# Optimization experiments

Hardware: AMD Instinct MI355X
Metric: run time of the kernel (lower is better)

## Reference

```python
import jax, jax.numpy as jnp
import numpy as np

NUM_USERS = 200000
NUM_ARTISTS = 50000
LATENT_DIM = 64
NUM_EDGES = 2000000
NUM_LAYERS = 3


def setup_inputs() -> dict:
    key = jax.random.key(0)
    k_u, k_a, k_src, k_dst = jax.random.split(key, 4)
    x_users = jax.random.normal(k_u, (NUM_USERS, LATENT_DIM), dtype=jnp.float32)
    x_artists = jax.random.normal(k_a, (NUM_ARTISTS, LATENT_DIM), dtype=jnp.float32)
    # a2u: row 0 = artist (source) ids, row 1 = user (target) ids
    art = jax.random.randint(k_src, (NUM_EDGES,), 0, NUM_ARTISTS, dtype=jnp.int32)
    usr = jax.random.randint(k_dst, (NUM_EDGES,), 0, NUM_USERS, dtype=jnp.int32)
    edge_index_a2u = jnp.stack([art, usr], axis=0)
    # u2a is the reversed edge list: row 0 = user (source), row 1 = artist (target)
    edge_index_u2a = jnp.stack([usr, art], axis=0)
    return {
        "x_users": x_users,
        "x_artists": x_artists,
        "edge_index_a2u": edge_index_a2u,
        "edge_index_u2a": edge_index_u2a,
    }


def _scatter_mean(src_nodes, edge_index, dim_size):
    """Gather src_nodes[edge_index[0]] and scatter-mean onto edge_index[1].

    Matches torch_scatter.scatter(reduce='mean'): empty segments yield 0.
    """
    msgs = src_nodes[edge_index[0]]                     # [E, D] gather
    sums = jax.ops.segment_sum(msgs, edge_index[1], num_segments=dim_size)
    ones = jnp.ones((edge_index.shape[1],), dtype=src_nodes.dtype)
    counts = jax.ops.segment_sum(ones, edge_index[1], num_segments=dim_size)
    return sums / jnp.maximum(counts, 1.0)[:, None]


def reference(x_users, x_artists, edge_index_a2u, edge_index_u2a):
    scale = 1.0 / (NUM_LAYERS + 1)
    final_u = x_users * scale
    final_a = x_artists * scale
    for _ in range(NUM_LAYERS):
        x_users = _scatter_mean(x_artists, edge_index_a2u, NUM_USERS)
        x_artists = _scatter_mean(x_users, edge_index_u2a, NUM_ARTISTS)
        final_u = final_u + x_users * scale
        final_a = final_a + x_artists * scale
    return final_u, final_a
```

## Files before the change

### kernel.cpp

```cpp
#include <hip/hip_runtime.h>
#include <hip/hip_fp16.h>

#define D 64
#define TB 256

#define BSHIFT_U 10
#define BSHIFT_A 8
#define CAP   12288
#define CAP_P 16384
#define SENT  0xFFFFFFFFu
#define TSHIFT 14

typedef _Float16 half8 __attribute__((ext_vector_type(8)));
typedef float float8 __attribute__((ext_vector_type(8)));
typedef float f32x4 __attribute__((ext_vector_type(4)));

__device__ __forceinline__ float8 h8_to_f8(half8 h) {
    return __builtin_convertvector(h, float8);
}
template <typename T>
__device__ __forceinline__ T ntl(const T* p) { return __builtin_nontemporal_load(p); }
template <typename T>
__device__ __forceinline__ void nts(T* p, T v) { __builtin_nontemporal_store(v, p); }

__global__ __launch_bounds__(TB) void cvt_f16_zero_kernel(const f32x4* __restrict__ in,
                                                          half8* __restrict__ out, int n8,
                                                          int* __restrict__ bcur, int nb) {
    int i = blockIdx.x * blockDim.x + threadIdx.x;
    int stride = gridDim.x * blockDim.x;
    for (int j = i; j < nb; j += stride) bcur[j] = 0;
    for (int j = i; j < n8; j += stride) {
        f32x4 a = in[j * 2 + 0];
        f32x4 b = in[j * 2 + 1];
        half8 h;
        h[0] = (_Float16)a[0]; h[1] = (_Float16)a[1]; h[2] = (_Float16)a[2]; h[3] = (_Float16)a[3];
        h[4] = (_Float16)b[0]; h[5] = (_Float16)b[1]; h[6] = (_Float16)b[2]; h[7] = (_Float16)b[3];
        out[j] = h;
    }
}

__global__ __launch_bounds__(TB) void partition_both_kernel(const int* __restrict__ art,
                                                            const int* __restrict__ usr, int E,
                                                            int* __restrict__ bcur_u,
                                                            int* __restrict__ bcur_a,
                                                            unsigned* __restrict__ part_u,
                                                            unsigned* __restrict__ part_a,
                                                            int NBu, int NBa) {
    __shared__ int cu[256], bu[256], ca[256], ba[256];
    for (int i = threadIdx.x; i < NBu; i += TB) cu[i] = 0;
    for (int i = threadIdx.x; i < NBa; i += TB) ca[i] = 0;
    __syncthreads();
    int chunk = (E + gridDim.x - 1) / gridDim.x;
    int e0 = blockIdx.x * chunk;
    int e1 = min(E, e0 + chunk);
    for (int e = e0 + threadIdx.x; e < e1; e += TB) {
        atomicAdd(&cu[usr[e] >> BSHIFT_U], 1);
        atomicAdd(&ca[art[e] >> BSHIFT_A], 1);
    }
    __syncthreads();
    for (int i = threadIdx.x; i < NBu; i += TB) {
        int c = cu[i];
        bu[i] = c ? (i * CAP_P + atomicAdd(&bcur_u[i], (c + 15) & ~15)) : 0;
        cu[i] = 0;
    }
    for (int i = threadIdx.x; i < NBa; i += TB) {
        int c = ca[i];
        ba[i] = c ? (i * CAP_P + atomicAdd(&bcur_a[i], (c + 15) & ~15)) : 0;
        ca[i] = 0;
    }
    __syncthreads();
    for (int e = e0 + threadIdx.x; e < e1; e += TB) {
        int a = art[e];
        int u = usr[e];
        int bui = u >> BSHIFT_U;
        int lu = atomicAdd(&cu[bui], 1);
        part_u[bu[bui] + lu] = ((unsigned)a << BSHIFT_U) | ((unsigned)u & ((1u << BSHIFT_U) - 1u));
        int bai = a >> BSHIFT_A;
        int la = atomicAdd(&ca[bai], 1);
        part_a[ba[bai] + la] = ((unsigned)u << BSHIFT_A) | ((unsigned)a & ((1u << BSHIFT_A) - 1u));
    }
    __syncthreads();
    for (int i = threadIdx.x; i < NBu; i += TB) {
        int c = cu[i];
        if (c) {
            int pad = (c + 15) & ~15;
            for (int k = c; k < pad; ++k) part_u[bu[i] + k] = SENT;
        }
    }
    for (int i = threadIdx.x; i < NBa; i += TB) {
        int c = ca[i];
        if (c) {
            int pad = (c + 15) & ~15;
            for (int k = c; k < pad; ++k) part_a[ba[i] + k] = SENT;
        }
    }
}

template <int NPB, int NB, int BSHIFT>
__device__ __forceinline__ void local_csr_body(const unsigned* __restrict__ part,
                                               int ecount, int ebeg_p, int ebeg_c, int n0,
                                               int2* __restrict__ rowdeg,
                                               int* __restrict__ csr, int N,
                                               int* cnt, int* sdata) {
    const int tid = threadIdx.x;
    const int NBINS = NPB * NB;
    const int eend = ebeg_p + ecount;
    const unsigned mask = (unsigned)(NPB - 1);
    for (int i = tid; i < NBINS; i += TB) cnt[i] = 0;
    __syncthreads();
    for (int e = ebeg_p + tid; e < eend; e += TB) {
        unsigned r = part[e];
        if (r != SENT) {
            int bin = (int)(r & mask) * NB + (int)((r >> BSHIFT) >> TSHIFT);
            atomicAdd(&cnt[bin], 1);
        }
    }
    __syncthreads();
    const int ITEMS = NBINS / TB;
    const int ib = tid * ITEMS;
    int local = 0;
    for (int k = 0; k < ITEMS; ++k) local += cnt[ib + k];
    sdata[tid] = local;
    __syncthreads();
    for (int off = 1; off < TB; off <<= 1) {
        int t = (tid >= off) ? sdata[tid - off] : 0;
        __syncthreads();
        if (tid >= off) sdata[tid] += t;
        __syncthreads();
    }
    int run = sdata[tid] - local;
    const int NPT = ITEMS / NB;
    for (int j = 0; j < NPT; ++j) {
        const int nodeStart = run;
        int d = 0;
        for (int k = 0; k < NB; ++k) {
            int idx = ib + j * NB + k;
            int v = cnt[idx];
            cnt[idx] = run;
            run += v;
            d += v;
        }
        int n = n0 + (ib / NB) + j;
        if (n < N) rowdeg[n] = make_int2(ebeg_c + nodeStart, d);
    }
    __syncthreads();
    for (int e = ebeg_p + tid; e < eend; e += TB) {
        unsigned r = part[e];
        if (r == SENT) continue;
        int bin = (int)(r & mask) * NB + (int)((r >> BSHIFT) >> TSHIFT);
        int pos = atomicAdd(&cnt[bin], 1);
        csr[ebeg_c + pos] = (int)(r >> BSHIFT);
    }
}

__global__ __launch_bounds__(TB) void local_csr_both_kernel(const unsigned* __restrict__ part_u,
                                                            const unsigned* __restrict__ part_a,
                                                            const int* __restrict__ bcur_u,
                                                            const int* __restrict__ bcur_a,
                                                            int2* __restrict__ rowdeg_u,
                                                            int2* __restrict__ rowdeg_a,
                                                            int* __restrict__ csr_u,
                                                            int* __restrict__ csr_a,
                                                            int NU, int NA, int NBu) {
    __shared__ int cnt[4096];
    __shared__ int sdata[TB];
    const int b = blockIdx.x;
    if (b < NBu) {
        local_csr_body<1024, 4, BSHIFT_U>(part_u, bcur_u[b], b * CAP_P, b * CAP,
                                          b << BSHIFT_U, rowdeg_u, csr_u, NU, cnt, sdata);
    } else {
        const int bb = b - NBu;
        local_csr_body<256, 16, BSHIFT_A>(part_a, bcur_a[bb], bb * CAP_P, bb * CAP,
                                          bb << BSHIFT_A, rowdeg_a, csr_a, NA, cnt, sdata);
    }
}

__global__ __launch_bounds__(TB) void gather_mean_kernel(const half8* __restrict__ src,
                                                         const int* __restrict__ csr,
                                                         const int2* __restrict__ rowdeg,
                                                         half8* __restrict__ x_out,
                                                         f32x4* __restrict__ final_acc,
                                                         const f32x4* __restrict__ init_src,
                                                         const f32x4* __restrict__ fin_in0,
                                                         const half8* __restrict__ fin_x1,
                                                         const half8* __restrict__ fin_x2,
                                                         f32x4* __restrict__ fin_out,
                                                         int N, float scale) {
    const int lane = threadIdx.x & 7;
    int g = (blockIdx.x * blockDim.x + threadIdx.x) >> 3;
    const int ngroups = (gridDim.x * blockDim.x) >> 3;
    for (int n = g; n < N; n += ngroups) {
        const int2 rd = rowdeg[n];
        const int beg = rd.x;
        const int dg = rd.y;
        const int end = beg + dg;
        float8 a0 = 0.f, a1 = 0.f, a2 = 0.f, a3 = 0.f;
        int e = beg;
        for (; e + 4 <= end; e += 4) {
            const int s0 = csr[e + 0];
            const int s1 = csr[e + 1];
            const int s2 = csr[e + 2];
            const int s3 = csr[e + 3];
            a0 += h8_to_f8(src[s0 * 8 + lane]);
            a1 += h8_to_f8(src[s1 * 8 + lane]);
            a2 += h8_to_f8(src[s2 * 8 + lane]);
            a3 += h8_to_f8(src[s3 * 8 + lane]);
        }
        for (; e < end; ++e)
            a0 += h8_to_f8(src[csr[e] * 8 + lane]);
        float8 s = (a0 + a1) + (a2 + a3);
        const float inv = 1.f / (float)(dg > 0 ? dg : 1);
        float8 x = s * inv;
        const int o8 = n * 8 + lane;
        if (x_out != nullptr) {
            half8 h;
            for (int k = 0; k < 8; ++k) h[k] = (_Float16)x[k];
            x_out[o8] = h;
        }
        const int fo = n * (D / 4) + lane * 2;
        if (fin_out != nullptr) {
            float8 t = h8_to_f8(ntl(&fin_x1[o8])) + h8_to_f8(ntl(&fin_x2[o8])) + x;
            f32x4 f0 = ntl(&fin_in0[fo + 0]);
            f32x4 f1 = ntl(&fin_in0[fo + 1]);
            f32x4 t0 = {t[0], t[1], t[2], t[3]};
            f32x4 t1 = {t[4], t[5], t[6], t[7]};
            nts(&fin_out[fo + 0], (f0 + t0) * scale);
            nts(&fin_out[fo + 1], (f1 + t1) * scale);
        }
        if (final_acc != nullptr) {
            f32x4 f0, f1;
            if (init_src != nullptr) {
                f0 = init_src[fo + 0] * scale;
                f1 = init_src[fo + 1] * scale;
            } else {
                f0 = final_acc[fo + 0];
                f1 = final_acc[fo + 1];
            }
            f32x4 x0 = {x[0], x[1], x[2], x[3]};
            f32x4 x1 = {x[4], x[5], x[6], x[7]};
            final_acc[fo + 0] = f0 + x0 * scale;
            final_acc[fo + 1] = f1 + x1 * scale;
        }
    }
}

extern "C" void kernel_launch(void* const* d_in, const int* in_sizes, int n_in,
                              void* d_out, int out_size, void* d_ws, size_t ws_size,
                              hipStream_t stream) {
    const float* x_users   = (const float*)d_in[0];
    const float* x_artists = (const float*)d_in[1];
    const int*   a2u       = (const int*)d_in[2];

    const int NU = in_sizes[0] / D;
    const int NA = in_sizes[1] / D;
    const int E  = in_sizes[2] / 2;
    const int* art = a2u;
    const int* usr = a2u + E;

    const float scale = 0.25f;

    const int NBu = (NU + (1 << BSHIFT_U) - 1) >> BSHIFT_U;
    const int NBa = (NA + (1 << BSHIFT_A) - 1) >> BSHIFT_A;

    char* w = (char*)d_ws;
    size_t off = 0;
    auto alloc = [&](size_t bytes) -> char* {
        char* p = w + off;
        off += (bytes + 255) & ~(size_t)255;
        return p;
    };
    int2* rowdeg_u = (int2*)alloc((size_t)NU * 8);
    int2* rowdeg_a = (int2*)alloc((size_t)NA * 8);
    int* bcur      = (int*)alloc((size_t)(NBu + NBa) * 4);
    int* bcur_u    = bcur;
    int* bcur_a    = bcur + NBu;
    int* csr_u     = (int*)alloc((size_t)NBu * CAP * 4);
    int* csr_a     = (int*)alloc((size_t)NBa * CAP * 4);
    half8* xa_in   = (half8*)alloc((size_t)NA * D * 2);
    unsigned* part_u = (unsigned*)alloc((size_t)NBu * CAP_P * 4);
    unsigned* part_a = (unsigned*)alloc((size_t)NBa * CAP_P * 4);

    const size_t XU = (size_t)NU * D * 2;
    const size_t XA = (size_t)NA * D * 2;
    const size_t XUa = (XU + 255) & ~(size_t)255;
    const size_t XAa = (XA + 255) & ~(size_t)255;

    const bool modeA = (off + 3 * XUa) <= ws_size;

    half8* x_u1 = (half8*)alloc(XU);
    half8* x_u2 = modeA ? (half8*)alloc(XU) : x_u1;
    half8* x_u3 = modeA ? (half8*)alloc(XU) : x_u1;
    char* part_base = (char*)part_u;
    half8* x_a1 = (half8*)(part_base);
    half8* x_a2 = modeA ? (half8*)(part_base + XAa) : x_a1;

    float* out_u = (float*)d_out;
    float* out_a = out_u + (size_t)NU * D;

    cvt_f16_zero_kernel<<<1024, TB, 0, stream>>>((const f32x4*)x_artists, xa_in,
                                                 NA * D / 8, bcur, NBu + NBa);
    partition_both_kernel<<<256, TB, 0, stream>>>(art, usr, E, bcur_u, bcur_a,
                                                  part_u, part_a, NBu, NBa);
    local_csr_both_kernel<<<NBu + NBa, TB, 0, stream>>>(part_u, part_a, bcur_u, bcur_a,
                                                        rowdeg_u, rowdeg_a,
                                                        csr_u, csr_a, NU, NA, NBu);

    half8* xu_buf[3] = {x_u1, x_u2, x_u3};
    half8* xa_buf[2] = {x_a1, x_a2};
    const half8* srcA = xa_in;
    for (int l = 0; l < 3; ++l) {
        const bool last = (l == 2);
        gather_mean_kernel<<<4096, TB, 0, stream>>>(
            srcA, csr_u, rowdeg_u, xu_buf[l],
            modeA ? nullptr : (f32x4*)out_u,
            (!modeA && l == 0) ? (const f32x4*)x_users : nullptr,
            (modeA && last) ? (const f32x4*)x_users : nullptr,
            (modeA && last) ? x_u1 : nullptr,
            (modeA && last) ? x_u2 : nullptr,
            (modeA && last) ? (f32x4*)out_u : nullptr,
            NU, scale);
        gather_mean_kernel<<<2048, TB, 0, stream>>>(
            xu_buf[l], csr_a, rowdeg_a,
            (modeA && last) ? nullptr : (modeA ? xa_buf[l] : x_a1),
            modeA ? nullptr : (f32x4*)out_a,
            (!modeA && l == 0) ? (const f32x4*)x_artists : nullptr,
            (modeA && last) ? (const f32x4*)x_artists : nullptr,
            (modeA && last) ? x_a1 : nullptr,
            (modeA && last) ? x_a2 : nullptr,
            (modeA && last) ? (f32x4*)out_a : nullptr,
            NA, scale);
        srcA = modeA ? xa_buf[l < 2 ? l : 0] : x_a1;
    }
}
```

Before: 359.2 us.

## Sort edges in shared memory before partitioning and pad CSR rows to multiples of four

The partition kernel now stages chunks of edges in LDS, counting-sorts them by bucket, and writes each bucket's run contiguously with coalesced stores. This replaces scattered per-edge global writes and sentinel padding. The local CSR build pads each row to a multiple of four with index-0 entries. The gather kernel then runs a branch-free 8-wide unrolled loop and subtracts the padding contribution using row 0's value. This adds LDS pressure, doubles the partition grid, and the subtraction introduces small fp rounding differences.

```diff
diff --git a/kernel.cpp b/kernel.cpp
--- a/kernel.cpp
+++ b/kernel.cpp
@@ -6,10 +6,11 @@
 
 #define BSHIFT_U 10
 #define BSHIFT_A 8
-#define CAP   12288
-#define CAP_P 16384
-#define SENT  0xFFFFFFFFu
+#define CAP    12288
+#define CAPC_U 16384
+#define CAPC_A 12288
 #define TSHIFT 14
+#define PCHUNK 4096
 
 typedef _Float16 half8 __attribute__((ext_vector_type(8)));
 typedef float float8 __attribute__((ext_vector_type(8)));
@@ -39,6 +40,55 @@
     }
 }
 
+struct PartShared {
+    unsigned recs[PCHUNK];
+    unsigned sorted[PCHUNK];
+    unsigned short loc[PCHUNK];
+    unsigned char bkt[PCHUNK];
+    int cnt[256];
+    int gbase[256];
+    int seg[256];
+    int scanbuf[TB];
+};
+
+__device__ __forceinline__ void part_direction(PartShared& sh, int m, int NB,
+                                               int* __restrict__ bcur,
+                                               unsigned* __restrict__ part) {
+    const int tid = threadIdx.x;
+    for (int i = tid; i < NB; i += TB) sh.cnt[i] = 0;
+    __syncthreads();
+    for (int i = tid; i < m; i += TB)
+        sh.loc[i] = (unsigned short)atomicAdd(&sh.cnt[sh.bkt[i]], 1);
+    __syncthreads();
+    int v = (tid < NB) ? sh.cnt[tid] : 0;
+    sh.scanbuf[tid] = v;
+    __syncthreads();
+    for (int off = 1; off < TB; off <<= 1) {
+        int t = (tid >= off) ? sh.scanbuf[tid - off] : 0;
+        __syncthreads();
+        if (tid >= off) sh.scanbuf[tid] += t;
+        __syncthreads();
+    }
+    if (tid < NB) {
+        sh.seg[tid] = sh.scanbuf[tid] - v;
+        if (v) sh.gbase[tid] = atomicAdd(&bcur[tid], v);
+    }
+    __syncthreads();
+    for (int i = tid; i < m; i += TB)
+        sh.sorted[sh.seg[sh.bkt[i]] + sh.loc[i]] = sh.recs[i];
+    __syncthreads();
+    const int wid = tid >> 6;
+    const int lane = tid & 63;
+    for (int b = wid; b < NB; b += TB / 64) {
+        int s = sh.seg[b];
+        int send = (b + 1 < NB) ? sh.seg[b + 1] : m;
+        if (send <= s) continue;
+        unsigned* dst = part + (size_t)b * CAP + sh.gbase[b];
+        for (int i = s + lane; i < send; i += 64) dst[i - s] = sh.sorted[i];
+    }
+    __syncthreads();
+}
+
 __global__ __launch_bounds__(TB) void partition_both_kernel(const int* __restrict__ art,
                                                             const int* __restrict__ usr, int E,
                                                             int* __restrict__ bcur_u,
@@ -46,53 +96,27 @@
                                                             unsigned* __restrict__ part_u,
                                                             unsigned* __restrict__ part_a,
                                                             int NBu, int NBa) {
-    __shared__ int cu[256], bu[256], ca[256], ba[256];
-    for (int i = threadIdx.x; i < NBu; i += TB) cu[i] = 0;
-    for (int i = threadIdx.x; i < NBa; i += TB) ca[i] = 0;
-    __syncthreads();
+    __shared__ PartShared sh;
+    const int tid = threadIdx.x;
     int chunk = (E + gridDim.x - 1) / gridDim.x;
     int e0 = blockIdx.x * chunk;
     int e1 = min(E, e0 + chunk);
-    for (int e = e0 + threadIdx.x; e < e1; e += TB) {
-        atomicAdd(&cu[usr[e] >> BSHIFT_U], 1);
-        atomicAdd(&ca[art[e] >> BSHIFT_A], 1);
-    }
-    __syncthreads();
-    for (int i = threadIdx.x; i < NBu; i += TB) {
-        int c = cu[i];
-        bu[i] = c ? (i * CAP_P + atomicAdd(&bcur_u[i], (c + 15) & ~15)) : 0;
-        cu[i] = 0;
-    }
-    for (int i = threadIdx.x; i < NBa; i += TB) {
-        int c = ca[i];
-        ba[i] = c ? (i * CAP_P + atomicAdd(&bcur_a[i], (c + 15) & ~15)) : 0;
-        ca[i] = 0;
-    }
-    __syncthreads();
-    for (int e = e0 + threadIdx.x; e < e1; e += TB) {
-        int a = art[e];
-        int u = usr[e];
-        int bui = u >> BSHIFT_U;
-        int lu = atomicAdd(&cu[bui], 1);
-        part_u[bu[bui] + lu] = ((unsigned)a << BSHIFT_U) | ((unsigned)u & ((1u << BSHIFT_U) - 1u));
-        int bai = a >> BSHIFT_A;
-        int la = atomicAdd(&ca[bai], 1);
-        part_a[ba[bai] + la] = ((unsigned)u << BSHIFT_A) | ((unsigned)a & ((1u << BSHIFT_A) - 1u));
-    }
-    __syncthreads();
-    for (int i = threadIdx.x; i < NBu; i += TB) {
-        int c = cu[i];
-        if (c) {
-            int pad = (c + 15) & ~15;
-            for (int k = c; k < pad; ++k) part_u[bu[i] + k] = SENT;
-        }
-    }
-    for (int i = threadIdx.x; i < NBa; i += TB) {
-        int c = ca[i];
-        if (c) {
-            int pad = (c + 15) & ~15;
-            for (int k = c; k < pad; ++k) part_a[ba[i] + k] = SENT;
-        }
+    for (int c0 = e0; c0 < e1; c0 += PCHUNK) {
+        int m = min(PCHUNK, e1 - c0);
+        for (int i = tid; i < m; i += TB) {
+            int a = art[c0 + i], u = usr[c0 + i];
+            sh.recs[i] = ((unsigned)a << BSHIFT_U) | ((unsigned)u & ((1u << BSHIFT_U) - 1u));
+            sh.bkt[i] = (unsigned char)(u >> BSHIFT_U);
+        }
+        __syncthreads();
+        part_direction(sh, m, NBu, bcur_u, part_u);
+        for (int i = tid; i < m; i += TB) {
+            int a = art[c0 + i], u = usr[c0 + i];
+            sh.recs[i] = ((unsigned)u << BSHIFT_A) | ((unsigned)a & ((1u << BSHIFT_A) - 1u));
+            sh.bkt[i] = (unsigned char)(a >> BSHIFT_A);
+        }
+        __syncthreads();
+        part_direction(sh, m, NBa, bcur_a, part_a);
     }
 }
 
@@ -110,16 +134,22 @@
     __syncthreads();
     for (int e = ebeg_p + tid; e < eend; e += TB) {
         unsigned r = part[e];
-        if (r != SENT) {
-            int bin = (int)(r & mask) * NB + (int)((r >> BSHIFT) >> TSHIFT);
-            atomicAdd(&cnt[bin], 1);
-        }
+        int bin = (int)(r & mask) * NB + (int)((r >> BSHIFT) >> TSHIFT);
+        atomicAdd(&cnt[bin], 1);
     }
     __syncthreads();
     const int ITEMS = NBINS / TB;
+    const int NPT = ITEMS / NB;
     const int ib = tid * ITEMS;
+    int dj[NPT], pdj[NPT], nsj[NPT];
     int local = 0;
-    for (int k = 0; k < ITEMS; ++k) local += cnt[ib + k];
+    for (int j = 0; j < NPT; ++j) {
+        int d = 0;
+        for (int k = 0; k < NB; ++k) d += cnt[ib + j * NB + k];
+        dj[j] = d;
+        pdj[j] = (d + 3) & ~3;
+        local += pdj[j];
+    }
     sdata[tid] = local;
     __syncthreads();
     for (int off = 1; off < TB; off <<= 1) {
@@ -129,28 +159,28 @@
         __syncthreads();
     }
     int run = sdata[tid] - local;
-    const int NPT = ITEMS / NB;
     for (int j = 0; j < NPT; ++j) {
-        const int nodeStart = run;
-        int d = 0;
+        nsj[j] = run;
+        int c = run;
         for (int k = 0; k < NB; ++k) {
             int idx = ib + j * NB + k;
             int v = cnt[idx];
-            cnt[idx] = run;
-            run += v;
-            d += v;
-        }
-        int n = n0 + (ib / NB) + j;
-        if (n < N) rowdeg[n] = make_int2(ebeg_c + nodeStart, d);
+            cnt[idx] = c;
+            c += v;
+        }
+        int n = n0 + tid * NPT + j;
+        if (n < N) rowdeg[n] = make_int2(ebeg_c + run, dj[j]);
+        run += pdj[j];
     }
     __syncthreads();
     for (int e = ebeg_p + tid; e < eend; e += TB) {
         unsigned r = part[e];
-        if (r == SENT) continue;
         int bin = (int)(r & mask) * NB + (int)((r >> BSHIFT) >> TSHIFT);
         int pos = atomicAdd(&cnt[bin], 1);
         csr[ebeg_c + pos] = (int)(r >> BSHIFT);
     }
+    for (int j = 0; j < NPT; ++j)
+        for (int k = dj[j]; k < pdj[j]; ++k) csr[ebeg_c + nsj[j] + k] = 0;
 }
 
 __global__ __launch_bounds__(TB) void local_csr_both_kernel(const unsigned* __restrict__ part_u,
@@ -166,11 +196,11 @@
     __shared__ int sdata[TB];
     const int b = blockIdx.x;
     if (b < NBu) {
-        local_csr_body<1024, 4, BSHIFT_U>(part_u, bcur_u[b], b * CAP_P, b * CAP,
+        local_csr_body<1024, 4, BSHIFT_U>(part_u, bcur_u[b], b * CAP, b * CAPC_U,
                                           b << BSHIFT_U, rowdeg_u, csr_u, NU, cnt, sdata);
     } else {
         const int bb = b - NBu;
-        local_csr_body<256, 16, BSHIFT_A>(part_a, bcur_a[bb], bb * CAP_P, bb * CAP,
+        local_csr_body<256, 16, BSHIFT_A>(part_a, bcur_a[bb], bb * CAP, bb * CAPC_A,
                                           bb << BSHIFT_A, rowdeg_a, csr_a, NA, cnt, sdata);
     }
 }
@@ -189,14 +219,42 @@
     const int lane = threadIdx.x & 7;
     int g = (blockIdx.x * blockDim.x + threadIdx.x) >> 3;
     const int ngroups = (gridDim.x * blockDim.x) >> 3;
+    const float8 r0 = h8_to_f8(src[lane]);
     for (int n = g; n < N; n += ngroups) {
         const int2 rd = rowdeg[n];
         const int beg = rd.x;
         const int dg = rd.y;
-        const int end = beg + dg;
+        const int pd = (dg + 3) & ~3;
+        const int end = beg + pd;
         float8 a0 = 0.f, a1 = 0.f, a2 = 0.f, a3 = 0.f;
         int e = beg;
-        for (; e + 4 <= end; e += 4) {
+        for (; e + 8 <= end; e += 8) {
+            const int s0 = csr[e + 0];
+            const int s1 = csr[e + 1];
+            const int s2 = csr[e + 2];
+            const int s3 = csr[e + 3];
+            const int s4 = csr[e + 4];
+            const int s5 = csr[e + 5];
+            const int s6 = csr[e + 6];
+            const int s7 = csr[e + 7];
+            const half8 v0 = src[s0 * 8 + lane];
+            const half8 v1 = src[s1 * 8 + lane];
+            const half8 v2 = src[s2 * 8 + lane];
+            const half8 v3 = src[s3 * 8 + lane];
+            const half8 v4 = src[s4 * 8 + lane];
+            const half8 v5 = src[s5 * 8 + lane];
+            const half8 v6 = src[s6 * 8 + lane];
+            const half8 v7 = src[s7 * 8 + lane];
+            a0 += h8_to_f8(v0);
+            a1 += h8_to_f8(v1);
+            a2 += h8_to_f8(v2);
+            a3 += h8_to_f8(v3);
+            a0 += h8_to_f8(v4);
+            a1 += h8_to_f8(v5);
+            a2 += h8_to_f8(v6);
+            a3 += h8_to_f8(v7);
+        }
+        if (e < end) {
             const int s0 = csr[e + 0];
             const int s1 = csr[e + 1];
             const int s2 = csr[e + 2];
@@ -206,9 +264,8 @@
             a2 += h8_to_f8(src[s2 * 8 + lane]);
             a3 += h8_to_f8(src[s3 * 8 + lane]);
         }
-        for (; e < end; ++e)
-            a0 += h8_to_f8(src[csr[e] * 8 + lane]);
         float8 s = (a0 + a1) + (a2 + a3);
+        s -= (float)(pd - dg) * r0;
         const float inv = 1.f / (float)(dg > 0 ? dg : 1);
         float8 x = s * inv;
         const int o8 = n * 8 + lane;
@@ -274,11 +331,11 @@
     int* bcur      = (int*)alloc((size_t)(NBu + NBa) * 4);
     int* bcur_u    = bcur;
     int* bcur_a    = bcur + NBu;
-    int* csr_u     = (int*)alloc((size_t)NBu * CAP * 4);
-    int* csr_a     = (int*)alloc((size_t)NBa * CAP * 4);
+    int* csr_u     = (int*)alloc((size_t)NBu * CAPC_U * 4);
+    int* csr_a     = (int*)alloc((size_t)NBa * CAPC_A * 4);
     half8* xa_in   = (half8*)alloc((size_t)NA * D * 2);
-    unsigned* part_u = (unsigned*)alloc((size_t)NBu * CAP_P * 4);
-    unsigned* part_a = (unsigned*)alloc((size_t)NBa * CAP_P * 4);
+    unsigned* part_u = (unsigned*)alloc((size_t)NBu * CAP * 4);
+    unsigned* part_a = (unsigned*)alloc((size_t)NBa * CAP * 4);
 
     const size_t XU = (size_t)NU * D * 2;
     const size_t XA = (size_t)NA * D * 2;
@@ -299,7 +356,7 @@
 
     cvt_f16_zero_kernel<<<1024, TB, 0, stream>>>((const f32x4*)x_artists, xa_in,
                                                  NA * D / 8, bcur, NBu + NBa);
-    partition_both_kernel<<<256, TB, 0, stream>>>(art, usr, E, bcur_u, bcur_a,
+    partition_both_kernel<<<512, TB, 0, stream>>>(art, usr, E, bcur_u, bcur_a,
                                                   part_u, part_a, NBu, NBa);
     local_csr_both_kernel<<<NBu + NBa, TB, 0, stream>>>(part_u, part_a, bcur_u, bcur_a,
                                                         rowdeg_u, rowdeg_a,
```

Measured after the change: 348.3 us. 1.03x faster.
